# Kernel tuning notes

Hardware: AMD Instinct MI355X
Metric: run time of the kernel (lower is better)

Reference implementation:

```python
import jax, jax.numpy as jnp
import numpy as np

EPS = 2.220446049250313e-16  # sys.float_info.epsilon
TEMP = 0.01

def maxpool2(x):
    b, c, h, w = x.shape
    return x.reshape(b, c, h // 2, 2, w // 2, 2).max(axis=(3, 5))

def conv1x1(x, w, b):
    # x: [B,C,H,W], w: [O,C], b: [O]
    return jnp.einsum('bchw,oc->bohw', x, w) + b[None, :, None, None]

def unfold3(x):
    # F.unfold(kernel_size=3, padding=1) -> [B, C*9, H*W], channel-major ordering
    b, c, h, w = x.shape
    xp = jnp.pad(x, ((0, 0), (0, 0), (1, 1), (1, 1)))
    patches = jnp.stack([xp[:, :, i:i + h, j:j + w] for i in range(3) for j in range(3)], axis=2)  # [b,c,9,h,w]
    return patches.reshape(b, c * 9, h * w)

def center_norm(t):
    # mean-center and L2-normalize over the patch-feature dim (dim=1)
    t = t - t.mean(axis=1, keepdims=True)
    return t / (jnp.linalg.norm(t, axis=1, keepdims=True) + EPS)

def setup_inputs() -> dict:
    key = jax.random.key(0)
    ks = jax.random.split(key, 12)
    B, C, H, W = 4, 256, 64, 64
    inp = {
        'block_fea': jax.random.normal(ks[0], (B, C, H, W), jnp.float32),
        'spp_input': jax.random.normal(ks[1], (B, C, H, W), jnp.float32),
        'click_map': jax.random.uniform(ks[2], (B, 2, H * 8, W * 8), jnp.float32),
        # click feature pyramid convs (1x1)
        'w1': jax.random.normal(ks[3], (64, 2), jnp.float32) * 0.1,
        'b1': jnp.zeros((64,), jnp.float32),
        'w2': jax.random.normal(ks[4], (128, 64), jnp.float32) * 0.05,
        'b2': jnp.zeros((128,), jnp.float32),
        'w3': jax.random.normal(ks[5], (256, 128), jnp.float32) * 0.05,
        'b3': jnp.zeros((256,), jnp.float32),
        # final cat conv: 512 -> 256
        'wc': jax.random.normal(ks[6], (256, 512), jnp.float32) * 0.03,
        'bc': jnp.zeros((256,), jnp.float32),
    }
    return inp

def reference(block_fea, spp_input, click_map, w1, b1, w2, b2, w3, b3, wc, bc):
    B, C, H, W = block_fea.shape
    HW = H * W
    # click feature: MaxPool-Conv x3 (2ch -> 64 -> 128 -> 256), spatial /8
    cf = conv1x1(maxpool2(click_map), w1, b1)
    cf = conv1x1(maxpool2(cf), w2, b2)
    cf = conv1x1(maxpool2(cf), w3, b3)  # [B,256,H,W]
    # get_corre: unfold + mean-center + L2-normalize (cosine similarity over 3x3 patches)
    theta = center_norm(unfold3(block_fea))  # [B, C*9, HW]
    # spp_input is already (H,W): bilinear interpolate to same size is identity
    phi = center_norm(unfold3(spp_input))    # [B, C*9, HW]
    f = jnp.einsum('bcm,bcn->bmn', theta, phi) / TEMP  # [B, HW, HW]
    f_div_C = jax.nn.softmax(f, axis=-1)
    # propagate: click_fea already (H,W) -> identity interpolate
    ref = cf.reshape(B, C, HW)
    y = jnp.einsum('bmn,bcn->bcm', f_div_C, ref).reshape(B, C, H, W)
    # upsample to (H,W) is identity; concat + 1x1 conv
    out = conv1x1(jnp.concatenate([block_fea, y], axis=1), wc, bc)
    return out
```

## Files before the change

### kernel.cpp

```cpp
#include <hip/hip_runtime.h>
#include <math.h>

#define EPSF 2.220446049250313e-16f

typedef short bf16x8 __attribute__((ext_vector_type(8)));
typedef float f32x4 __attribute__((ext_vector_type(4)));

static __device__ __forceinline__ unsigned short f2bf(float x) {
  union { float f; unsigned u; } v; v.f = x;
  unsigned r = v.u + 0x7fffu + ((v.u >> 16) & 1u);
  return (unsigned short)(r >> 16);
}

__global__ __launch_bounds__(256) void k_zero(float* __restrict__ p) {
  const int t = blockIdx.x * 256 + threadIdx.x;
  float4 z = make_float4(0.f, 0.f, 0.f, 0.f);
  *reinterpret_cast<float4*>(&p[(size_t)t * 4]) = z;
}

__global__ __launch_bounds__(256) void k_wsplit(const float* __restrict__ wc,
    unsigned short* __restrict__ wcLb, unsigned short* __restrict__ wcRb) {
  const int idx = blockIdx.x * 256 + threadIdx.x;
  const int o = idx >> 9, k = idx & 511;
  const float v = wc[idx];
  if (k < 256) wcLb[o * 256 + k] = f2bf(v);
  else         wcRb[o * 256 + (k - 256)] = f2bf(v);
}

__global__ __launch_bounds__(256) void k_tcast(const float* __restrict__ src0,
    unsigned short* __restrict__ dst0, int R, int C,
    size_t src_z, size_t dst_z, float* __restrict__ SA, float* __restrict__ QA) {
  __shared__ float ld[64][65];
  const float* src = src0 + blockIdx.z * src_z;
  unsigned short* dst = dst0 + blockIdx.z * dst_z;
  const int c0 = blockIdx.x * 64, r0 = blockIdx.y * 64;
  const int t = threadIdx.x;
  const int colr = t & 63, rowr = t >> 6;
  float s = 0.f, q = 0.f;
  #pragma unroll
  for (int i = 0; i < 16; ++i) {
    const int rl = rowr + i * 4;
    const float v = src[(size_t)(r0 + rl) * C + c0 + colr];
    ld[colr][rl] = v;
    s += v; q += v * v;
  }
  if (SA) {
    atomicAdd(&SA[blockIdx.z * 4096 + c0 + colr], s);
    atomicAdd(&QA[blockIdx.z * 4096 + c0 + colr], q);
  }
  __syncthreads();
  const int rl = t & 63, clb = t >> 6;
  #pragma unroll
  for (int i = 0; i < 16; ++i) {
    const int cl = clb + i * 4;
    dst[(size_t)(c0 + cl) * R + r0 + rl] = f2bf(ld[cl][rl]);
  }
}

__global__ __launch_bounds__(128) void k_pyr1(const float* __restrict__ click,
    const float* __restrict__ w1, const float* __restrict__ b1,
    const float* __restrict__ w2, const float* __restrict__ b2,
    float* __restrict__ cf2) {
  __shared__ float pool1[16][8];
  __shared__ float pooled64[16][64];
  const int b = blockIdx.y;
  const int pg = blockIdx.x;
  const int tid = threadIdx.x;
  {
    const int q = tid >> 3, s = (tid >> 1) & 3, c = tid & 1;
    const int p2 = pg * 16 + q;
    const int y2 = p2 >> 7, x2 = p2 & 127;
    const int sy = s >> 1, sx = s & 1;
    const int row = 4 * y2 + 2 * sy, col = 4 * x2 + 2 * sx;
    const float* base = click + (((size_t)(b * 2 + c)) * 512 + row) * 512 + col;
    pool1[q][s * 2 + c] = fmaxf(fmaxf(base[0], base[1]), fmaxf(base[512], base[513]));
  }
  __syncthreads();
  {
    const int c1 = tid & 63, qh = tid >> 6;
    const float wa = w1[c1 * 2], wb = w1[c1 * 2 + 1], bb = b1[c1];
    #pragma unroll
    for (int r = 0; r < 8; ++r) {
      const int q = qh * 8 + r;
      float v = -3.4e38f;
      #pragma unroll
      for (int s = 0; s < 4; ++s)
        v = fmaxf(v, bb + wa * pool1[q][s * 2] + wb * pool1[q][s * 2 + 1]);
      pooled64[q][c1] = v;
    }
  }
  __syncthreads();
  float acc[16];
  #pragma unroll
  for (int q = 0; q < 16; ++q) acc[q] = b2[tid];
  const float4* wrow = reinterpret_cast<const float4*>(w2 + tid * 64);
  #pragma unroll
  for (int k4 = 0; k4 < 16; ++k4) {
    const float4 w = wrow[k4];
    #pragma unroll
    for (int q = 0; q < 16; ++q) {
      const float4 p = *reinterpret_cast<const float4*>(&pooled64[q][k4 * 4]);
      acc[q] += w.x * p.x + w.y * p.y + w.z * p.z + w.w * p.w;
    }
  }
  #pragma unroll
  for (int q = 0; q < 16; ++q)
    cf2[((size_t)b * 16384 + pg * 16 + q) * 128 + tid] = acc[q];
}

__global__ __launch_bounds__(256) void k_pyr2(const float* __restrict__ cf2,
    const float* __restrict__ w3, const float* __restrict__ b3,
    unsigned short* __restrict__ cf3b) {
  __shared__ float pooled[16][128];
  const int b = blockIdx.y;
  const int pb = blockIdx.x;
  const int tid = threadIdx.x;
  #pragma unroll
  for (int i = 0; i < 8; ++i) {
    const int idx = tid + 256 * i;
    const int q = idx >> 7, c = idx & 127;
    const int p = pb * 16 + q;
    const int y = p >> 6, x = p & 63;
    const size_t r0 = (size_t)b * 16384 + (2 * y) * 128 + 2 * x;
    const float* s0 = cf2 + r0 * 128 + c;
    pooled[q][c] = fmaxf(fmaxf(s0[0], s0[128]), fmaxf(s0[128 * 128], s0[128 * 129]));
  }
  __syncthreads();
  float acc[16];
  #pragma unroll
  for (int q = 0; q < 16; ++q) acc[q] = b3[tid];
  const float4* wrow = reinterpret_cast<const float4*>(w3 + tid * 128);
  #pragma unroll
  for (int k4 = 0; k4 < 32; ++k4) {
    const float4 w = wrow[k4];
    #pragma unroll
    for (int q = 0; q < 16; ++q) {
      const float4 p = *reinterpret_cast<const float4*>(&pooled[q][k4 * 4]);
      acc[q] += w.x * p.x + w.y * p.y + w.z * p.z + w.w * p.w;
    }
  }
  #pragma unroll
  for (int q = 0; q < 16; ++q)
    cf3b[((size_t)b * 4096 + pb * 16 + q) * 256 + tid] = f2bf(acc[q]);
}

__global__ __launch_bounds__(256) void k_stats9(const float* __restrict__ SA,
    const float* __restrict__ QA, const float* __restrict__ SB, const float* __restrict__ QB,
    float* __restrict__ muA, float* __restrict__ invA,
    float* __restrict__ muB, float* __restrict__ invB) {
  const int b = blockIdx.y;
  const int m = blockIdx.x * 256 + threadIdx.x;
  const int y = m >> 6, x = m & 63;
  const int base = b * 4096;
  float sa = 0, qa = 0, sb = 0, qb = 0;
  #pragma unroll
  for (int dy = -1; dy <= 1; ++dy) {
    const int yy = y + dy;
    if ((unsigned)yy >= 64u) continue;
    #pragma unroll
    for (int dx = -1; dx <= 1; ++dx) {
      const int xx = x + dx;
      if ((unsigned)xx >= 64u) continue;
      const int idx = base + yy * 64 + xx;
      sa += SA[idx]; qa += QA[idx];
      sb += SB[idx]; qb += QB[idx];
    }
  }
  const float ma = sa * (1.f / 2304.f);
  const float mb = sb * (1.f / 2304.f);
  const float na = sqrtf(fmaxf(qa - 2304.f * ma * ma, 0.f));
  const float nb = sqrtf(fmaxf(qb - 2304.f * mb * mb, 0.f));
  muA[base + m] = ma;
  invA[base + m] = 1.f / (na + EPSF);
  muB[base + m] = mb;
  invB[base + m] = 1.f / (nb + EPSF);
}

#define ROWP 40
static __device__ __forceinline__ void stage_tile(const unsigned short* __restrict__ src,
    size_t srow, int r0, int k0, unsigned short* __restrict__ lds, int tid) {
  #pragma unroll
  for (int p = 0; p < 2; ++p) {
    const int idx = tid + p * 256;
    const int m = idx >> 2, q = idx & 3;
    const bf16x8 v = *reinterpret_cast<const bf16x8*>(src + (size_t)(r0 + m) * srow + k0 + q * 8);
    *reinterpret_cast<bf16x8*>(lds + m * ROWP + q * 8) = v;
  }
}

static __device__ __forceinline__ bf16x8 frag(const unsigned short* __restrict__ lds,
                                              int row, int q) {
  return *reinterpret_cast<const bf16x8*>(lds + row * ROWP + q * 8);
}

__global__ __launch_bounds__(256) void k_gemm_g(const unsigned short* __restrict__ At,
    const unsigned short* __restrict__ Bt, float* __restrict__ G) {
  __shared__ unsigned short As[128 * ROWP];
  __shared__ unsigned short Bs[128 * ROWP];
  const int tid = threadIdx.x;
  const int lin = blockIdx.y * 32 + blockIdx.x;
  const int nlin = ((lin & 7) << 7) | (lin >> 3);
  const int m0 = (nlin >> 5) * 128, n0 = (nlin & 31) * 128;
  const int l = tid & 63, w = tid >> 6;
  const int wr = w >> 1, wc = w & 1;
  const int q = l >> 4, lr = l & 15;
  f32x4 acc[4][4];
  #pragma unroll
  for (int i = 0; i < 4; ++i)
    #pragma unroll
    for (int j = 0; j < 4; ++j)
      acc[i][j] = f32x4{0.f, 0.f, 0.f, 0.f};
  for (int k0 = 0; k0 < 256; k0 += 32) {
    stage_tile(At, 256, m0, k0, As, tid);
    stage_tile(Bt, 256, n0, k0, Bs, tid);
    __syncthreads();
    bf16x8 a[4], bvv[4];
    #pragma unroll
    for (int i = 0; i < 4; ++i) a[i] = frag(As, wr * 64 + i * 16 + lr, q);
    #pragma unroll
    for (int j = 0; j < 4; ++j) bvv[j] = frag(Bs, wc * 64 + j * 16 + lr, q);
    #pragma unroll
    for (int i = 0; i < 4; ++i)
      #pragma unroll
      for (int j = 0; j < 4; ++j)
        acc[i][j] = __builtin_amdgcn_mfma_f32_16x16x32_bf16(a[i], bvv[j], acc[i][j], 0, 0, 0);
    __syncthreads();
  }
  const int rb = 4 * q;
  #pragma unroll
  for (int i = 0; i < 4; ++i)
    #pragma unroll
    for (int j = 0; j < 4; ++j) {
      const size_t base = (size_t)(m0 + wr * 64 + i * 16 + rb) * 4096 + n0 + wc * 64 + j * 16 + lr;
      #pragma unroll
      for (int r = 0; r < 4; ++r)
        G[base + (size_t)r * 4096] = acc[i][j][r];
    }
}

__global__ __launch_bounds__(256) void k_gemm_cf2(const unsigned short* __restrict__ wcRb,
    const unsigned short* __restrict__ cf3b, unsigned short* __restrict__ CF2t) {
  __shared__ unsigned short As[128 * ROWP];
  __shared__ unsigned short Bs[128 * ROWP];
  const int b = blockIdx.z;
  const int tid = threadIdx.x;
  const int o0 = blockIdx.y * 128, n0 = blockIdx.x * 128;
  const unsigned short* Bb = cf3b + (size_t)b * 4096 * 256;
  unsigned short* outb = CF2t + (size_t)b * 256 * 4096;
  const int l = tid & 63, w = tid >> 6;
  const int wr = w >> 1, wcol = w & 1;
  const int q = l >> 4, lr = l & 15;
  f32x4 acc[4][4];
  #pragma unroll
  for (int i = 0; i < 4; ++i)
    #pragma unroll
    for (int j = 0; j < 4; ++j)
      acc[i][j] = f32x4{0.f, 0.f, 0.f, 0.f};
  for (int k0 = 0; k0 < 256; k0 += 32) {
    stage_tile(wcRb, 256, o0, k0, As, tid);
    stage_tile(Bb, 256, n0, k0, Bs, tid);
    __syncthreads();
    bf16x8 a[4], bvv[4];
    #pragma unroll
    for (int i = 0; i < 4; ++i) a[i] = frag(As, wr * 64 + i * 16 + lr, q);
    #pragma unroll
    for (int j = 0; j < 4; ++j) bvv[j] = frag(Bs, wcol * 64 + j * 16 + lr, q);
    #pragma unroll
    for (int i = 0; i < 4; ++i)
      #pragma unroll
      for (int j = 0; j < 4; ++j)
        acc[i][j] = __builtin_amdgcn_mfma_f32_16x16x32_bf16(a[i], bvv[j], acc[i][j], 0, 0, 0);
    __syncthreads();
  }
  const int rb = 4 * q;
  #pragma unroll
  for (int i = 0; i < 4; ++i)
    #pragma unroll
    for (int j = 0; j < 4; ++j) {
      const size_t base = (size_t)(o0 + wr * 64 + i * 16 + rb) * 4096 + n0 + wcol * 64 + j * 16 + lr;
      #pragma unroll
      for (int r = 0; r < 4; ++r)
        outb[base + (size_t)r * 4096] = f2bf(acc[i][j][r]);
    }
}

__global__ __launch_bounds__(256) void k_gemm_oinit(const unsigned short* __restrict__ wcLb,
    const unsigned short* __restrict__ At, const float* __restrict__ bc,
    float* __restrict__ OUT) {
  __shared__ unsigned short As[128 * ROWP];
  __shared__ unsigned short Bs[128 * ROWP];
  const int b = blockIdx.z;
  const int tid = threadIdx.x;
  const int o0 = blockIdx.y * 128, m0 = blockIdx.x * 128;
  const unsigned short* Bb = At + (size_t)b * 4096 * 256;
  float* outb = OUT + (size_t)b * 256 * 4096;
  const int l = tid & 63, w = tid >> 6;
  const int wr = w >> 1, wcol = w & 1;
  const int q = l >> 4, lr = l & 15;
  f32x4 acc[4][4];
  #pragma unroll
  for (int i = 0; i < 4; ++i)
    #pragma unroll
    for (int j = 0; j < 4; ++j)
      acc[i][j] = f32x4{0.f, 0.f, 0.f, 0.f};
  for (int k0 = 0; k0 < 256; k0 += 32) {
    stage_tile(wcLb, 256, o0, k0, As, tid);
    stage_tile(Bb, 256, m0, k0, Bs, tid);
    __syncthreads();
    bf16x8 a[4], bvv[4];
    #pragma unroll
    for (int i = 0; i < 4; ++i) a[i] = frag(As, wr * 64 + i * 16 + lr, q);
    #pragma unroll
    for (int j = 0; j < 4; ++j) bvv[j] = frag(Bs, wcol * 64 + j * 16 + lr, q);
    #pragma unroll
    for (int i = 0; i < 4; ++i)
      #pragma unroll
      for (int j = 0; j < 4; ++j)
        acc[i][j] = __builtin_amdgcn_mfma_f32_16x16x32_bf16(a[i], bvv[j], acc[i][j], 0, 0, 0);
    __syncthreads();
  }
  const int rb = 4 * q;
  #pragma unroll
  for (int i = 0; i < 4; ++i)
    #pragma unroll
    for (int j = 0; j < 4; ++j) {
      #pragma unroll
      for (int r = 0; r < 4; ++r) {
        const int o = o0 + wr * 64 + i * 16 + rb + r;
        outb[(size_t)o * 4096 + m0 + wcol * 64 + j * 16 + lr] = acc[i][j][r] + bc[o];
      }
    }
}

__global__ __launch_bounds__(256) void k_fsoft(const float* __restrict__ G,
    const float* __restrict__ muA, const float* __restrict__ invA,
    const float* __restrict__ muB, const float* __restrict__ invB,
    unsigned short* __restrict__ P) {
  __shared__ float redm[4];
  __shared__ float reds[4];
  const int m = ((blockIdx.x & 7) << 9) | (blockIdx.x >> 3);
  const int tid = threadIdx.x;
  const int ym = m >> 6, xm = m & 63;
  const int xn = tid & 63, ty = tid >> 6;

  const float* base[9];
  bool xok[9];
  #pragma unroll
  for (int dy = -1; dy <= 1; ++dy) {
    #pragma unroll
    for (int dx = -1; dx <= 1; ++dx) {
      const int g = (dy + 1) * 3 + (dx + 1);
      const bool rv = ((unsigned)(ym + dy) < 64u) && ((unsigned)(xm + dx) < 64u);
      const int d = dy * 64 + dx;
      base[g] = rv ? (G + (size_t)(m + d) * 4096 + d) : G;
      xok[g] = rv && ((unsigned)(xn + dx) < 64u);
    }
  }

  float acc[16];
  #pragma unroll
  for (int u = 0; u < 16; ++u) acc[u] = 0.f;

  #pragma unroll
  for (int uc = 0; uc < 4; ++uc) {
    float v[36];
    #pragma unroll
    for (int g = 0; g < 9; ++g) {
      #pragma unroll
      for (int r = 0; r < 4; ++r) {
        const int u = uc * 4 + r;
        v[g * 4 + r] = base[g][u * 256 + tid];
      }
    }
    #pragma unroll
    for (int g = 0; g < 9; ++g) {
      const int dy = g / 3 - 1;
      #pragma unroll
      for (int r = 0; r < 4; ++r) {
        const int u = uc * 4 + r;
        const bool ok = xok[g] && ((unsigned)(4 * u + ty + dy) < 64u);
        acc[u] += ok ? v[g * 4 + r] : 0.f;
      }
    }
  }

  const float s1 = 2304.f * muA[m];
  const float ia100 = invA[m] * 100.f;
  float mx = -3.4e38f;
  #pragma unroll
  for (int u = 0; u < 16; ++u) {
    const int n = tid + u * 256;
    const float lg = (acc[u] - s1 * muB[n]) * (ia100 * invB[n]);
    acc[u] = lg;
    mx = fmaxf(mx, lg);
  }
  #pragma unroll
  for (int off = 32; off; off >>= 1) mx = fmaxf(mx, __shfl_xor(mx, off));
  const int wave = tid >> 6, lane = tid & 63;
  if (lane == 0) redm[wave] = mx;
  __syncthreads();
  mx = fmaxf(fmaxf(redm[0], redm[1]), fmaxf(redm[2], redm[3]));
  float s = 0.f;
  #pragma unroll
  for (int u = 0; u < 16; ++u) {
    acc[u] = __expf(acc[u] - mx);
    s += acc[u];
  }
  #pragma unroll
  for (int off = 32; off; off >>= 1) s += __shfl_xor(s, off);
  if (lane == 0) reds[wave] = s;
  __syncthreads();
  s = reds[0] + reds[1] + reds[2] + reds[3];
  const float inv = 1.f / s;
  unsigned short* row = P + (size_t)m * 4096;
  #pragma unroll
  for (int u = 0; u < 16; ++u)
    row[tid + u * 256] = f2bf(acc[u] * inv);
}

__global__ __launch_bounds__(256) void k_pv(const unsigned short* __restrict__ CF2t,
    const unsigned short* __restrict__ P, float* __restrict__ OUT) {
  __shared__ unsigned short As[128 * ROWP];
  __shared__ unsigned short Bs[128 * ROWP];
  const int tid = threadIdx.x;
  const int c0 = blockIdx.y * 128, mb0 = blockIdx.x * 128;
  const int kbase = blockIdx.z * 512;
  const int l = tid & 63, w = tid >> 6;
  const int wr = w >> 1, wc = w & 1;
  const int q = l >> 4, lr = l & 15;
  f32x4 acc[4][4];
  #pragma unroll
  for (int i = 0; i < 4; ++i)
    #pragma unroll
    for (int j = 0; j < 4; ++j)
      acc[i][j] = f32x4{0.f, 0.f, 0.f, 0.f};
  for (int ks = 0; ks < 512; ks += 32) {
    const int k0 = kbase + ks;
    stage_tile(CF2t, 4096, c0, k0, As, tid);
    stage_tile(P, 4096, mb0, k0, Bs, tid);
    __syncthreads();
    bf16x8 a[4], bvv[4];
    #pragma unroll
    for (int i = 0; i < 4; ++i) a[i] = frag(As, wr * 64 + i * 16 + lr, q);
    #pragma unroll
    for (int j = 0; j < 4; ++j) bvv[j] = frag(Bs, wc * 64 + j * 16 + lr, q);
    #pragma unroll
    for (int i = 0; i < 4; ++i)
      #pragma unroll
      for (int j = 0; j < 4; ++j)
        acc[i][j] = __builtin_amdgcn_mfma_f32_16x16x32_bf16(a[i], bvv[j], acc[i][j], 0, 0, 0);
    __syncthreads();
  }
  const int rb = 4 * q;
  #pragma unroll
  for (int i = 0; i < 4; ++i)
    #pragma unroll
    for (int j = 0; j < 4; ++j) {
      #pragma unroll
      for (int r = 0; r < 4; ++r) {
        const size_t o = (size_t)(c0 + wr * 64 + i * 16 + rb + r) * 4096 + mb0 + wc * 64 + j * 16 + lr;
        atomicAdd(&OUT[o], acc[i][j][r]);
      }
    }
}

extern "C" void kernel_launch(void* const* d_in, const int* in_sizes, int n_in,
                              void* d_out, int out_size, void* d_ws, size_t ws_size,
                              hipStream_t stream) {
  const float* block_fea = (const float*)d_in[0];
  const float* spp       = (const float*)d_in[1];
  const float* click     = (const float*)d_in[2];
  const float* w1 = (const float*)d_in[3];
  const float* b1 = (const float*)d_in[4];
  const float* w2 = (const float*)d_in[5];
  const float* b2 = (const float*)d_in[6];
  const float* w3 = (const float*)d_in[7];
  const float* b3 = (const float*)d_in[8];
  const float* wc = (const float*)d_in[9];
  const float* bc = (const float*)d_in[10];
  float* out = (float*)d_out;

  float* ws = (float*)d_ws;
  const size_t M1 = 1024 * 1024;
  float* cf2  = ws;
  float* G    = ws + 256;
  unsigned short* Pb   = (unsigned short*)(ws + 17 * M1);
  unsigned short* At   = (unsigned short*)(ws + 25 * M1);
  unsigned short* Bt   = (unsigned short*)(ws + 27 * M1);
  unsigned short* CF3b = (unsigned short*)(ws + 29 * M1);
  unsigned short* CF2t = (unsigned short*)(ws + 31 * M1);
  unsigned short* wcLb = (unsigned short*)(ws + 35 * M1);
  unsigned short* wcRb = wcLb + 65536;
  float* SA   = ws + 36 * M1;
  float* QA   = SA + 16384;
  float* SB   = QA + 16384;
  float* QB   = SB + 16384;
  float* muA  = QB + 16384;
  float* invA = muA + 16384;
  float* muB  = invA + 16384;
  float* invB = muB + 16384;

  k_zero<<<dim3(64), 256, 0, stream>>>(SA);
  k_wsplit<<<dim3(512), 256, 0, stream>>>(wc, wcLb, wcRb);
  k_pyr1<<<dim3(1024, 4), 128, 0, stream>>>(click, w1, b1, w2, b2, cf2);
  k_pyr2<<<dim3(256, 4), 256, 0, stream>>>(cf2, w3, b3, CF3b);
  k_tcast<<<dim3(64, 4, 4), 256, 0, stream>>>(block_fea, At, 256, 4096,
                                              (size_t)256 * 4096, (size_t)4096 * 256, SA, QA);
  k_tcast<<<dim3(64, 4, 4), 256, 0, stream>>>(spp, Bt, 256, 4096,
                                              (size_t)256 * 4096, (size_t)4096 * 256, SB, QB);
  k_stats9<<<dim3(16, 4), 256, 0, stream>>>(SA, QA, SB, QB, muA, invA, muB, invB);
  k_gemm_cf2<<<dim3(32, 2, 4), 256, 0, stream>>>(wcRb, CF3b, CF2t);
  k_gemm_oinit<<<dim3(32, 2, 4), 256, 0, stream>>>(wcLb, At, bc, out);

  for (int b = 0; b < 4; ++b) {
    const unsigned short* Atb = At + (size_t)b * 4096 * 256;
    const unsigned short* Btb = Bt + (size_t)b * 4096 * 256;
    k_gemm_g<<<dim3(32, 32), 256, 0, stream>>>(Atb, Btb, G);
    k_fsoft<<<dim3(4096), 256, 0, stream>>>(G, muA + b * 4096, invA + b * 4096,
                                            muB + b * 4096, invB + b * 4096, Pb);
    k_pv<<<dim3(32, 2, 8), 256, 0, stream>>>(CF2t + (size_t)b * 256 * 4096, Pb,
                                             out + (size_t)b * 256 * 4096);
  }
}
```

Measured before the change: 574.8 us.

## Double-buffer LDS tiles with register prefetch in all MFMA GEMM kernels

```diff
diff --git a/kernel.cpp b/kernel.cpp
--- a/kernel.cpp
+++ b/kernel.cpp
@@ -177,26 +177,74 @@
 }
 
 #define ROWP 40
-static __device__ __forceinline__ void stage_tile(const unsigned short* __restrict__ src,
-    size_t srow, int r0, int k0, unsigned short* __restrict__ lds, int tid) {
-  #pragma unroll
-  for (int p = 0; p < 2; ++p) {
-    const int idx = tid + p * 256;
-    const int m = idx >> 2, q = idx & 3;
-    const bf16x8 v = *reinterpret_cast<const bf16x8*>(src + (size_t)(r0 + m) * srow + k0 + q * 8);
-    *reinterpret_cast<bf16x8*>(lds + m * ROWP + q * 8) = v;
-  }
-}
-
 static __device__ __forceinline__ bf16x8 frag(const unsigned short* __restrict__ lds,
                                               int row, int q) {
   return *reinterpret_cast<const bf16x8*>(lds + row * ROWP + q * 8);
 }
+static __device__ __forceinline__ bf16x8 ldg8(const unsigned short* p) {
+  return *reinterpret_cast<const bf16x8*>(p);
+}
+
+static __device__ __forceinline__ void mfma_dbuf(
+    const unsigned short* __restrict__ Aop, size_t sA, int ra0,
+    const unsigned short* __restrict__ Bop, size_t sB, int rb0,
+    int k0, int nk,
+    unsigned short* As0, unsigned short* As1,
+    unsigned short* Bs0, unsigned short* Bs1,
+    int tid, f32x4 (&acc)[4][4]) {
+  const int l = tid & 63, w = tid >> 6;
+  const int wr = w >> 1, wcc = w & 1;
+  const int q = l >> 4, lr = l & 15;
+  const int rr = tid >> 2, qq = tid & 3;
+  const unsigned short* pa0 = Aop + (size_t)(ra0 + rr) * sA + qq * 8 + k0;
+  const unsigned short* pa1 = Aop + (size_t)(ra0 + 64 + rr) * sA + qq * 8 + k0;
+  const unsigned short* pb0 = Bop + (size_t)(rb0 + rr) * sB + qq * 8 + k0;
+  const unsigned short* pb1 = Bop + (size_t)(rb0 + 64 + rr) * sB + qq * 8 + k0;
+  const int wo0 = rr * ROWP + qq * 8;
+  const int wo1 = (64 + rr) * ROWP + qq * 8;
+  *reinterpret_cast<bf16x8*>(As0 + wo0) = ldg8(pa0);
+  *reinterpret_cast<bf16x8*>(As0 + wo1) = ldg8(pa1);
+  *reinterpret_cast<bf16x8*>(Bs0 + wo0) = ldg8(pb0);
+  *reinterpret_cast<bf16x8*>(Bs0 + wo1) = ldg8(pb1);
+  __syncthreads();
+  unsigned short *Ac = As0, *An = As1, *Bc = Bs0, *Bn = Bs1;
+  for (int t = 0; t < nk; ++t) {
+    const bool more = (t + 1) < nk;
+    const int kk = (t + 1) * 32;
+    bf16x8 na0, na1, nb0, nb1;
+    if (more) {
+      na0 = ldg8(pa0 + kk);
+      na1 = ldg8(pa1 + kk);
+      nb0 = ldg8(pb0 + kk);
+      nb1 = ldg8(pb1 + kk);
+    }
+    bf16x8 a[4], bv[4];
+    #pragma unroll
+    for (int i = 0; i < 4; ++i) a[i] = frag(Ac, wr * 64 + i * 16 + lr, q);
+    #pragma unroll
+    for (int j = 0; j < 4; ++j) bv[j] = frag(Bc, wcc * 64 + j * 16 + lr, q);
+    #pragma unroll
+    for (int i = 0; i < 4; ++i)
+      #pragma unroll
+      for (int j = 0; j < 4; ++j)
+        acc[i][j] = __builtin_amdgcn_mfma_f32_16x16x32_bf16(a[i], bv[j], acc[i][j], 0, 0, 0);
+    if (more) {
+      *reinterpret_cast<bf16x8*>(An + wo0) = na0;
+      *reinterpret_cast<bf16x8*>(An + wo1) = na1;
+      *reinterpret_cast<bf16x8*>(Bn + wo0) = nb0;
+      *reinterpret_cast<bf16x8*>(Bn + wo1) = nb1;
+    }
+    __syncthreads();
+    unsigned short* tp;
+    tp = Ac; Ac = An; An = tp;
+    tp = Bc; Bc = Bn; Bn = tp;
+  }
+}
 
 __global__ __launch_bounds__(256) void k_gemm_g(const unsigned short* __restrict__ At,
     const unsigned short* __restrict__ Bt, float* __restrict__ G) {
-  __shared__ unsigned short As[128 * ROWP];
-  __shared__ unsigned short Bs[128 * ROWP];
+  __shared__ unsigned short As[2][128 * ROWP];
+  __shared__ unsigned short Bs[2][128 * ROWP];
   const int tid = threadIdx.x;
   const int lin = blockIdx.y * 32 + blockIdx.x;
   const int nlin = ((lin & 7) << 7) | (lin >> 3);
@@ -210,22 +258,7 @@
     #pragma unroll
     for (int j = 0; j < 4; ++j)
       acc[i][j] = f32x4{0.f, 0.f, 0.f, 0.f};
-  for (int k0 = 0; k0 < 256; k0 += 32) {
-    stage_tile(At, 256, m0, k0, As, tid);
-    stage_tile(Bt, 256, n0, k0, Bs, tid);
-    __syncthreads();
-    bf16x8 a[4], bvv[4];
-    #pragma unroll
-    for (int i = 0; i < 4; ++i) a[i] = frag(As, wr * 64 + i * 16 + lr, q);
-    #pragma unroll
-    for (int j = 0; j < 4; ++j) bvv[j] = frag(Bs, wc * 64 + j * 16 + lr, q);
-    #pragma unroll
-    for (int i = 0; i < 4; ++i)
-      #pragma unroll
-      for (int j = 0; j < 4; ++j)
-        acc[i][j] = __builtin_amdgcn_mfma_f32_16x16x32_bf16(a[i], bvv[j], acc[i][j], 0, 0, 0);
-    __syncthreads();
-  }
+  mfma_dbuf(At, 256, m0, Bt, 256, n0, 0, 8, As[0], As[1], Bs[0], Bs[1], tid, acc);
   const int rb = 4 * q;
   #pragma unroll
   for (int i = 0; i < 4; ++i)
@@ -240,8 +273,8 @@
 
 __global__ __launch_bounds__(256) void k_gemm_cf2(const unsigned short* __restrict__ wcRb,
     const unsigned short* __restrict__ cf3b, unsigned short* __restrict__ CF2t) {
-  __shared__ unsigned short As[128 * ROWP];
-  __shared__ unsigned short Bs[128 * ROWP];
+  __shared__ unsigned short As[2][128 * ROWP];
+  __shared__ unsigned short Bs[2][128 * ROWP];
   const int b = blockIdx.z;
   const int tid = threadIdx.x;
   const int o0 = blockIdx.y * 128, n0 = blockIdx.x * 128;
@@ -256,22 +289,7 @@
     #pragma unroll
     for (int j = 0; j < 4; ++j)
       acc[i][j] = f32x4{0.f, 0.f, 0.f, 0.f};
-  for (int k0 = 0; k0 < 256; k0 += 32) {
-    stage_tile(wcRb, 256, o0, k0, As, tid);
-    stage_tile(Bb, 256, n0, k0, Bs, tid);
-    __syncthreads();
-    bf16x8 a[4], bvv[4];
-    #pragma unroll
-    for (int i = 0; i < 4; ++i) a[i] = frag(As, wr * 64 + i * 16 + lr, q);
-    #pragma unroll
-    for (int j = 0; j < 4; ++j) bvv[j] = frag(Bs, wcol * 64 + j * 16 + lr, q);
-    #pragma unroll
-    for (int i = 0; i < 4; ++i)
-      #pragma unroll
-      for (int j = 0; j < 4; ++j)
-        acc[i][j] = __builtin_amdgcn_mfma_f32_16x16x32_bf16(a[i], bvv[j], acc[i][j], 0, 0, 0);
-    __syncthreads();
-  }
+  mfma_dbuf(wcRb, 256, o0, Bb, 256, n0, 0, 8, As[0], As[1], Bs[0], Bs[1], tid, acc);
   const int rb = 4 * q;
   #pragma unroll
   for (int i = 0; i < 4; ++i)
@@ -287,8 +305,8 @@
 __global__ __launch_bounds__(256) void k_gemm_oinit(const unsigned short* __restrict__ wcLb,
     const unsigned short* __restrict__ At, const float* __restrict__ bc,
     float* __restrict__ OUT) {
-  __shared__ unsigned short As[128 * ROWP];
-  __shared__ unsigned short Bs[128 * ROWP];
+  __shared__ unsigned short As[2][128 * ROWP];
+  __shared__ unsigned short Bs[2][128 * ROWP];
   const int b = blockIdx.z;
   const int tid = threadIdx.x;
   const int o0 = blockIdx.y * 128, m0 = blockIdx.x * 128;
@@ -303,22 +321,7 @@
     #pragma unroll
     for (int j = 0; j < 4; ++j)
       acc[i][j] = f32x4{0.f, 0.f, 0.f, 0.f};
-  for (int k0 = 0; k0 < 256; k0 += 32) {
-    stage_tile(wcLb, 256, o0, k0, As, tid);
-    stage_tile(Bb, 256, m0, k0, Bs, tid);
-    __syncthreads();
-    bf16x8 a[4], bvv[4];
-    #pragma unroll
-    for (int i = 0; i < 4; ++i) a[i] = frag(As, wr * 64 + i * 16 + lr, q);
-    #pragma unroll
-    for (int j = 0; j < 4; ++j) bvv[j] = frag(Bs, wcol * 64 + j * 16 + lr, q);
-    #pragma unroll
-    for (int i = 0; i < 4; ++i)
-      #pragma unroll
-      for (int j = 0; j < 4; ++j)
-        acc[i][j] = __builtin_amdgcn_mfma_f32_16x16x32_bf16(a[i], bvv[j], acc[i][j], 0, 0, 0);
-    __syncthreads();
-  }
+  mfma_dbuf(wcLb, 256, o0, Bb, 256, m0, 0, 8, As[0], As[1], Bs[0], Bs[1], tid, acc);
   const int rb = 4 * q;
   #pragma unroll
   for (int i = 0; i < 4; ++i)
@@ -420,8 +423,8 @@
 
 __global__ __launch_bounds__(256) void k_pv(const unsigned short* __restrict__ CF2t,
     const unsigned short* __restrict__ P, float* __restrict__ OUT) {
-  __shared__ unsigned short As[128 * ROWP];
-  __shared__ unsigned short Bs[128 * ROWP];
+  __shared__ unsigned short As[2][128 * ROWP];
+  __shared__ unsigned short Bs[2][128 * ROWP];
   const int tid = threadIdx.x;
   const int c0 = blockIdx.y * 128, mb0 = blockIdx.x * 128;
   const int kbase = blockIdx.z * 512;
@@ -434,23 +437,7 @@
     #pragma unroll
     for (int j = 0; j < 4; ++j)
       acc[i][j] = f32x4{0.f, 0.f, 0.f, 0.f};
-  for (int ks = 0; ks < 512; ks += 32) {
-    const int k0 = kbase + ks;
-    stage_tile(CF2t, 4096, c0, k0, As, tid);
-    stage_tile(P, 4096, mb0, k0, Bs, tid);
-    __syncthreads();
-    bf16x8 a[4], bvv[4];
-    #pragma unroll
-    for (int i = 0; i < 4; ++i) a[i] = frag(As, wr * 64 + i * 16 + lr, q);
-    #pragma unroll
-    for (int j = 0; j < 4; ++j) bvv[j] = frag(Bs, wc * 64 + j * 16 + lr, q);
-    #pragma unroll
-    for (int i = 0; i < 4; ++i)
-      #pragma unroll
-      for (int j = 0; j < 4; ++j)
-        acc[i][j] = __builtin_amdgcn_mfma_f32_16x16x32_bf16(a[i], bvv[j], acc[i][j], 0, 0, 0);
-    __syncthreads();
-  }
+  mfma_dbuf(CF2t, 4096, c0, P, 4096, mb0, kbase, 16, As[0], As[1], Bs[0], Bs[1], tid, acc);
   const int rb = 4 * q;
   #pragma unroll
   for (int i = 0; i < 4; ++i)
```

After: 555.4 us. 3.4% less time.
